# Optimization experiments

Hardware: AMD Instinct MI355X
Metric: run time of the kernel (lower is better)

Reference implementation:

```python
import jax, jax.numpy as jnp
import numpy as np

B, L, D, H, MAXREL = 8, 1024, 1024, 16, 32
DPH = D // H  # 64


def setup_inputs() -> dict:
    rng = jax.random.key(0)
    ks = jax.random.split(rng, 16)
    s = 0.02
    inp = {
        "key": jax.random.normal(ks[0], (B, L, D), jnp.float32),
        "value": jax.random.normal(ks[1], (B, L, D), jnp.float32),
        "query": jax.random.normal(ks[2], (B, L, D), jnp.float32),
        "mask": jax.random.bernoulli(ks[3], 0.1, (B, 1, L)),
        "Wq": jax.random.normal(ks[4], (D, D), jnp.float32) * s,
        "bq": jnp.zeros((D,), jnp.float32),
        "Wk": jax.random.normal(ks[5], (D, D), jnp.float32) * s,
        "bk": jnp.zeros((D,), jnp.float32),
        "Wv": jax.random.normal(ks[6], (D, D), jnp.float32) * s,
        "bv": jnp.zeros((D,), jnp.float32),
        "Wo": jax.random.normal(ks[7], (D, D), jnp.float32) * s,
        "bo": jnp.zeros((D,), jnp.float32),
        "rel_emb": jax.random.normal(ks[8], (2 * MAXREL + 1, DPH), jnp.float32) * s,
    }
    return inp


def reference(key, value, query, mask, Wq, bq, Wk, bk, Wv, bv, Wo, bo, rel_emb):
    b, l, d = query.shape
    def shape(x):  # (b, l, D) -> (b, H, l, dph)
        return x.reshape(b, -1, H, DPH).transpose(0, 2, 1, 3)

    q = shape(query @ Wq.T + bq) / jnp.sqrt(jnp.asarray(DPH, query.dtype))
    k = shape(key @ Wk.T + bk)
    v = shape(value @ Wv.T + bv)

    # Shaw-style relative position embeddings: rel[i, j] = clip(j - i, -M, M) + M
    idx = jnp.arange(l)
    rel = jnp.clip(idx[None, :] - idx[:, None], -MAXREL, MAXREL) + MAXREL  # (l, l)
    Er = rel_emb[rel]  # (l, l, dph) -- used for both keys and values (same table)

    scores = jnp.einsum('bhqd,bhkd->bhqk', q, k) + jnp.einsum('bhqd,qkd->bhqk', q, Er)
    scores = jnp.where(mask[:, None, :, :], jnp.asarray(-1e18, scores.dtype), scores)
    attn = jax.nn.softmax(scores, axis=-1)  # dropout = identity at eval

    ctx = jnp.einsum('bhqk,bhkd->bhqd', attn, v) + jnp.einsum('bhqk,qkd->bhqd', attn, Er)
    out = ctx.transpose(0, 2, 1, 3).reshape(b, l, H * DPH) @ Wo.T + bo
    top_attn = attn[:, 0]  # (b, q_len, k_len)
    return out, top_attn
```

## Files before the change

### kernel.cpp

```cpp
#include <hip/hip_runtime.h>
#include <hip/hip_bf16.h>

typedef __bf16 bf16x8 __attribute__((ext_vector_type(8)));
typedef __bf16 bf16x4 __attribute__((ext_vector_type(4)));
typedef float f32x4 __attribute__((ext_vector_type(4)));
typedef float f32x8 __attribute__((ext_vector_type(8)));

#define B_ 8
#define L_ 1024
#define D_ 1024
#define H_ 16
#define DPH_ 64
#define MAXREL_ 32
#define NREL_ 65

__device__ __forceinline__ f32x4 mfma16x16x32(bf16x8 a, bf16x8 b, f32x4 c) {
    return __builtin_amdgcn_mfma_f32_16x16x32_bf16(a, b, c, 0, 0, 0);
}

__device__ __forceinline__ bf16x8 ld_any(const float* p) {
    f32x8 v = *(const f32x8*)p;
    bf16x8 r;
    #pragma unroll
    for (int i = 0; i < 8; ++i) r[i] = (__bf16)v[i];
    return r;
}
__device__ __forceinline__ bf16x8 ld_any(const __bf16* p) { return *(const bf16x8*)p; }

template <int MODE, typename TA>
__global__ __launch_bounds__(256) void gemm128(
    const TA* __restrict__ X, const float* __restrict__ Wt,
    const float* __restrict__ bias, void* __restrict__ outp,
    int M, int N, int K, float scale)
{
    __shared__ __bf16 sA[128 * 64];
    __shared__ __bf16 sB[128 * 64];

    const int tid = threadIdx.x;
    const int nbn = N >> 7;
    const int nwg = (M >> 7) * nbn;
    const int wg  = ((int)blockIdx.x & 7) * (nwg >> 3) + ((int)blockIdx.x >> 3);
    const int row0 = (wg / nbn) * 128, col0 = (wg % nbn) * 128;
    const int lane = tid & 63, w = tid >> 6, lr = lane & 15, lk = lane >> 4;
    const int wm = w >> 1, wn = w & 1;
    const int srow = tid >> 3;
    const int schk = tid & 7;

    bf16x8 ra[4], rb[4];
    f32x4 acc[4][4];
    #pragma unroll
    for (int a = 0; a < 4; ++a)
        #pragma unroll
        for (int b = 0; b < 4; ++b) acc[a][b] = (f32x4){0.f, 0.f, 0.f, 0.f};

    const int nkt = K >> 6;
    {
        const int kc = schk * 8;
        #pragma unroll
        for (int u = 0; u < 4; ++u) {
            const int r = u * 32 + srow;
            ra[u] = ld_any(X  + (size_t)(row0 + r) * K + kc);
            rb[u] = ld_any(Wt + (size_t)(col0 + r) * K + kc);
        }
    }
    for (int kt = 0; kt < nkt; ++kt) {
        __syncthreads();
        #pragma unroll
        for (int u = 0; u < 4; ++u) {
            const int r = u * 32 + srow;
            *(bf16x8*)&sA[r * 64 + ((schk ^ (r & 7)) * 8)] = ra[u];
            *(bf16x8*)&sB[r * 64 + ((schk ^ (r & 7)) * 8)] = rb[u];
        }
        __syncthreads();
        if (kt + 1 < nkt) {
            const int kc = (kt + 1) * 64 + schk * 8;
            #pragma unroll
            for (int u = 0; u < 4; ++u) {
                const int r = u * 32 + srow;
                ra[u] = ld_any(X  + (size_t)(row0 + r) * K + kc);
                rb[u] = ld_any(Wt + (size_t)(col0 + r) * K + kc);
            }
        }
        #pragma unroll
        for (int kk = 0; kk < 2; ++kk) {
            bf16x8 af[4], bf[4];
            #pragma unroll
            for (int mi = 0; mi < 4; ++mi) {
                const int r = wm * 64 + mi * 16 + lr;
                af[mi] = *(const bf16x8*)&sA[r * 64 + (((kk * 4 + lk) ^ (r & 7)) * 8)];
            }
            #pragma unroll
            for (int ni = 0; ni < 4; ++ni) {
                const int r = wn * 64 + ni * 16 + lr;
                bf[ni] = *(const bf16x8*)&sB[r * 64 + (((kk * 4 + lk) ^ (r & 7)) * 8)];
            }
            #pragma unroll
            for (int mi = 0; mi < 4; ++mi)
                #pragma unroll
                for (int ni = 0; ni < 4; ++ni)
                    acc[mi][ni] = mfma16x16x32(af[mi], bf[ni], acc[mi][ni]);
        }
    }

    #pragma unroll
    for (int ni = 0; ni < 4; ++ni) {
        const int n = col0 + wn * 64 + ni * 16 + lr;
        const float bv = bias[n];
        #pragma unroll
        for (int mi = 0; mi < 4; ++mi) {
            const int m0 = row0 + wm * 64 + mi * 16 + lk * 4;
            if (MODE == 0) {
                #pragma unroll
                for (int i = 0; i < 4; ++i)
                    ((__bf16*)outp)[(size_t)(m0 + i) * N + n] =
                        (__bf16)((acc[mi][ni][i] + bv) * scale);
            } else if (MODE == 1) {
                bf16x4 v4;
                #pragma unroll
                for (int i = 0; i < 4; ++i) v4[i] = (__bf16)(acc[mi][ni][i] + bv);
                *(bf16x4*)((__bf16*)outp + ((size_t)(m0 >> 10) << 20)
                           + (size_t)n * L_ + (m0 & 1023)) = v4;
            } else {
                #pragma unroll
                for (int i = 0; i < 4; ++i)
                    ((float*)outp)[(size_t)(m0 + i) * N + n] = acc[mi][ni][i] + bv;
            }
        }
    }
}

__global__ __launch_bounds__(256, 3) void attn_v5(
    const __bf16* __restrict__ Q, const __bf16* __restrict__ K,
    const __bf16* __restrict__ Vt, const int* __restrict__ mask,
    const float* __restrict__ relg, __bf16* __restrict__ ctx,
    float* __restrict__ attn0)
{
    __shared__ __bf16 sK[2][64 * 64];
    __shared__ __bf16 sV[2][64 * 64];
    __shared__ __bf16 s_rq[64 * 72];
    __shared__ __bf16 s_arel[64 * 72];
    __shared__ float s_sums[64];
    __shared__ unsigned s_mbits[32];

    const int tid = threadIdx.x;
    const int wg = ((int)blockIdx.x & 7) * 256 + ((int)blockIdx.x >> 3);
    const int qt = wg & 15, h = (wg >> 4) & 15, b = wg >> 8;
    const int q0 = qt * 64;
    const int lane = tid & 63, w = tid >> 6, lr = lane & 15, lk = lane >> 4;
    const size_t bh = (size_t)b * (L_ * D_) + (size_t)h * DPH_;
    const int qw = q0 + w * 16;
    const int ql = w * 16;

    const int strow = tid >> 3;
    const int scg   = (tid & 7) ^ (strow & 7);
    const __bf16* Kgp = K + bh + (size_t)strow * D_ + scg * 8;
    const __bf16* Vgp = Vt + ((size_t)b << 20)
                      + (size_t)(h * DPH_ + strow) * L_ + scg * 8;

    const __bf16* qp = Q + bh + (size_t)(qw + lr) * D_ + 8 * lk;
    const bf16x8 qf0 = *(const bf16x8*)qp;
    const bf16x8 qf1 = *(const bf16x8*)(qp + 32);

    #pragma unroll
    for (int rr = 0; rr < 4; ++rr) {
        const int k = rr * 256 + w * 64 + lane;
        const unsigned long long bal = __ballot(mask[b * L_ + k] != 0);
        if (lane == 0) {
            s_mbits[rr * 8 + w * 2]     = (unsigned)bal;
            s_mbits[rr * 8 + w * 2 + 1] = (unsigned)(bal >> 32);
        }
    }
    for (int i = tid; i < 64 * 72; i += 256) s_arel[i] = (__bf16)0.f;

    #pragma unroll
    for (int jt = 0; jt < 5; ++jt) {
        const int jr = jt * 16 + lr;
        const int jc = jr > 64 ? 64 : jr;
        const float* rp = relg + jc * 64 + 8 * lk;
        f32x4 rq = {0.f, 0.f, 0.f, 0.f};
        rq = mfma16x16x32(ld_any(rp), qf0, rq);
        rq = mfma16x16x32(ld_any(rp + 32), qf1, rq);
        #pragma unroll
        for (int i = 0; i < 4; ++i) {
            const int jj = jt * 16 + lk * 4 + i;
            if (jj <= 64) s_rq[(ql + lr) * 72 + jj] = (__bf16)rq[i];
        }
    }

    bf16x8 rk0 = *(const bf16x8*)(Kgp);
    bf16x8 rk1 = *(const bf16x8*)(Kgp + 32 * (size_t)D_);
    bf16x8 rv0 = *(const bf16x8*)(Vgp);
    bf16x8 rv1 = *(const bf16x8*)(Vgp + 32 * (size_t)L_);
    __syncthreads();

    const float rq0  = (float)s_rq[(ql + lr) * 72 + 0];
    const float rq64 = (float)s_rq[(ql + lr) * 72 + 64];

    float sum = 0.f, c0 = 0.f, c64 = 0.f;
    f32x4 pvacc[4];
    #pragma unroll
    for (int dt = 0; dt < 4; ++dt) pvacc[dt] = (f32x4){0.f, 0.f, 0.f, 0.f};
    float* a0p = attn0 + ((size_t)b * L_ + qw + lr) * L_;
    const int sw = lr & 7;
    const int s0l = lr + 32 * (lk & 1);
    const int s1l = s0l + 16;
    const bool hisel = (lk >> 1) != 0;

    for (int it = 0; it < 16; ++it) {
        const int cur = it & 1;
        const int k0 = it * 64;
        {
            __bf16* kd = &sK[cur][tid * 8];
            __bf16* vd = &sV[cur][tid * 8];
            *(bf16x8*)kd = rk0;  *(bf16x8*)(kd + 2048) = rk1;
            *(bf16x8*)vd = rv0;  *(bf16x8*)(vd + 2048) = rv1;
        }
        __syncthreads();
        if (it < 15) {
            const size_t ko = (size_t)(k0 + 64) * D_;
            rk0 = *(const bf16x8*)(Kgp + ko);
            rk1 = *(const bf16x8*)(Kgp + ko + 32 * (size_t)D_);
            rv0 = *(const bf16x8*)(Vgp + k0 + 64);
            rv1 = *(const bf16x8*)(Vgp + k0 + 64 + 32 * (size_t)L_);
        }

        const __bf16* kb = sK[cur];
        const __bf16* vb = sV[cur];

        float p[4][4];
        #pragma unroll
        for (int kt = 0; kt < 4; ++kt) {
            const int rb = (kt * 16 + lr) * 64;
            const bf16x8 a0 = *(const bf16x8*)&kb[rb + ((lk ^ sw) * 8)];
            const bf16x8 a1 = *(const bf16x8*)&kb[rb + (((lk + 4) ^ sw) * 8)];
            f32x4 acc = {0.f, 0.f, 0.f, 0.f};
            acc = mfma16x16x32(a0, qf0, acc);
            acc = mfma16x16x32(a1, qf1, acc);
            #pragma unroll
            for (int i = 0; i < 4; ++i) p[kt][i] = acc[i];
        }

        const unsigned mw0 = s_mbits[(k0 >> 5)];
        const unsigned mw1 = s_mbits[(k0 >> 5) + 1];
        const int side = (k0 <= qw - 95) ? -1 : ((k0 >= qw + 47) ? 1 : 0);
        if (side == 0) {
            #pragma unroll
            for (int kt = 0; kt < 4; ++kt) {
                const unsigned mword = kt < 2 ? mw0 : mw1;
                #pragma unroll
                for (int i = 0; i < 4; ++i) {
                    const int k = k0 + kt * 16 + lk * 4 + i;
                    const int dd = k - (qw + lr);
                    int j = dd + MAXREL_;
                    j = j < 0 ? 0 : (j > 64 ? 64 : j);
                    const float bias = (float)s_rq[(ql + lr) * 72 + j];
                    const float e = ((mword >> (k & 31)) & 1u)
                                  ? 0.f : __expf(p[kt][i] + bias);
                    p[kt][i] = e;
                    sum += e;
                    if (dd <= -MAXREL_)      c0  += e;
                    else if (dd >= MAXREL_)  c64 += e;
                    else s_arel[(ql + lr) * 72 + dd + MAXREL_] = (__bf16)e;
                }
            }
        } else {
            const float bias = side < 0 ? rq0 : rq64;
            float cacc = 0.f;
            #pragma unroll
            for (int kt = 0; kt < 4; ++kt) {
                const unsigned mword = kt < 2 ? mw0 : mw1;
                #pragma unroll
                for (int i = 0; i < 4; ++i) {
                    const int k = k0 + kt * 16 + lk * 4 + i;
                    const float e = ((mword >> (k & 31)) & 1u)
                                  ? 0.f : __expf(p[kt][i] + bias);
                    p[kt][i] = e;
                    cacc += e;
                }
            }
            sum += cacc;
            if (side < 0) c0 += cacc; else c64 += cacc;
        }

        if (h == 0) {
            #pragma unroll
            for (int kt = 0; kt < 4; ++kt) {
                f32x4 st;
                #pragma unroll
                for (int i = 0; i < 4; ++i) st[i] = p[kt][i];
                *(f32x4*)&a0p[k0 + kt * 16 + lk * 4] = st;
            }
        }

        unsigned pk[4][2];
        #pragma unroll
        for (int kt = 0; kt < 4; ++kt)
            #pragma unroll
            for (int hf = 0; hf < 2; ++hf) {
                union { unsigned u; __bf16 x[2]; } t;
                t.x[0] = (__bf16)p[kt][2 * hf];
                t.x[1] = (__bf16)p[kt][2 * hf + 1];
                pk[kt][hf] = t.u;
            }

        #pragma unroll
        for (int s = 0; s < 2; ++s) {
            union { unsigned u[4]; bf16x8 v; } ua;
            {
                const unsigned aE0 = __shfl((int)pk[2 * s][0],     s0l, 64);
                const unsigned aO0 = __shfl((int)pk[2 * s + 1][0], s0l, 64);
                const unsigned aE1 = __shfl((int)pk[2 * s][1],     s0l, 64);
                const unsigned aO1 = __shfl((int)pk[2 * s + 1][1], s0l, 64);
                const unsigned bE0 = __shfl((int)pk[2 * s][0],     s1l, 64);
                const unsigned bO0 = __shfl((int)pk[2 * s + 1][0], s1l, 64);
                const unsigned bE1 = __shfl((int)pk[2 * s][1],     s1l, 64);
                const unsigned bO1 = __shfl((int)pk[2 * s + 1][1], s1l, 64);
                ua.u[0] = hisel ? aO0 : aE0;
                ua.u[1] = hisel ? aO1 : aE1;
                ua.u[2] = hisel ? bO0 : bE0;
                ua.u[3] = hisel ? bO1 : bE1;
            }
            #pragma unroll
            for (int dt = 0; dt < 4; ++dt) {
                const bf16x8 bfv = *(const bf16x8*)
                    &vb[(dt * 16 + lr) * 64 + (((4 * s + lk) ^ sw) * 8)];
                pvacc[dt] = mfma16x16x32(ua.v, bfv, pvacc[dt]);
            }
        }
    }

    sum += __shfl_xor(sum, 16, 64); sum += __shfl_xor(sum, 32, 64);
    c0  += __shfl_xor(c0, 16, 64);  c0  += __shfl_xor(c0, 32, 64);
    c64 += __shfl_xor(c64, 16, 64); c64 += __shfl_xor(c64, 32, 64);
    if (lane < 16) {
        s_sums[ql + lr] = sum;
        s_arel[(ql + lr) * 72 + 0]  = (__bf16)c0;
        s_arel[(ql + lr) * 72 + 64] = (__bf16)c64;
    }
    __syncthreads();

    __bf16* rT = (__bf16*)sK;
    for (int i = tid; i < NREL_ * DPH_; i += 256)
        rT[(i & 63) * 72 + (i >> 6)] = (__bf16)relg[i];
    __syncthreads();

    const bf16x8 af1 = *(const bf16x8*)&s_arel[(ql + lr) * 72 + 8 * lk];
    const bf16x8 af2 = *(const bf16x8*)&s_arel[(ql + lr) * 72 + 32 + 8 * lk];
    float a64[4], inv[4];
    #pragma unroll
    for (int i = 0; i < 4; ++i) {
        a64[i] = (float)s_arel[(ql + lk * 4 + i) * 72 + 64];
        inv[i] = 1.f / s_sums[ql + lk * 4 + i];
    }
    #pragma unroll
    for (int dt = 0; dt < 4; ++dt) {
        const bf16x8 b1 = *(const bf16x8*)&rT[(dt * 16 + lr) * 72 + 8 * lk];
        const bf16x8 b2 = *(const bf16x8*)&rT[(dt * 16 + lr) * 72 + 32 + 8 * lk];
        pvacc[dt] = mfma16x16x32(af1, b1, pvacc[dt]);
        pvacc[dt] = mfma16x16x32(af2, b2, pvacc[dt]);
        const float r64 = (float)rT[(dt * 16 + lr) * 72 + 64];
        #pragma unroll
        for (int i = 0; i < 4; ++i) {
            const float outv = (pvacc[dt][i] + a64[i] * r64) * inv[i];
            ctx[((size_t)b * L_ + q0 + ql + lk * 4 + i) * D_
                + h * DPH_ + dt * 16 + lr] = (__bf16)outv;
        }
    }

    if (h == 0) {
        #pragma unroll 4
        for (int n = 0; n < 16; ++n) {
            const float invr = 1.f / s_sums[ql + n];
            float* ap = attn0 + ((size_t)b * L_ + q0 + ql + n) * L_ + lane * 16;
            #pragma unroll
            for (int c = 0; c < 4; ++c) {
                f32x4 v = *(f32x4*)&ap[c * 4];
                #pragma unroll
                for (int i = 0; i < 4; ++i) v[i] *= invr;
                *(f32x4*)&ap[c * 4] = v;
            }
        }
    }
}

extern "C" void kernel_launch(void* const* d_in, const int* in_sizes, int n_in,
                              void* d_out, int out_size, void* d_ws, size_t ws_size,
                              hipStream_t stream) {
    const float* key   = (const float*)d_in[0];
    const float* value = (const float*)d_in[1];
    const float* query = (const float*)d_in[2];
    const int*   mask  = (const int*)d_in[3];
    const float* Wq = (const float*)d_in[4];
    const float* bq = (const float*)d_in[5];
    const float* Wk = (const float*)d_in[6];
    const float* bk = (const float*)d_in[7];
    const float* Wv = (const float*)d_in[8];
    const float* bv = (const float*)d_in[9];
    const float* Wo = (const float*)d_in[10];
    const float* bo = (const float*)d_in[11];
    const float* relg = (const float*)d_in[12];

    float* out   = (float*)d_out;
    float* attn0 = out + (size_t)B_ * L_ * D_;

    char* ws = (char*)d_ws;
    __bf16* Qw   = (__bf16*)(ws);
    __bf16* Kw   = (__bf16*)(ws + ((size_t)16 << 20));
    __bf16* Vtw  = (__bf16*)(ws + ((size_t)32 << 20));
    __bf16* Ctxw = (__bf16*)(ws + ((size_t)48 << 20));

    const dim3 blk(256);
    const int M = B_ * L_;
    const int ngemm = (M / 128) * (D_ / 128);

    gemm128<0, float><<<ngemm, blk, 0, stream>>>(query, Wq, bq, Qw, M, D_, D_, 0.125f);
    gemm128<0, float><<<ngemm, blk, 0, stream>>>(key,   Wk, bk, Kw, M, D_, D_, 1.0f);
    gemm128<1, float><<<ngemm, blk, 0, stream>>>(value, Wv, bv, Vtw, M, D_, D_, 1.0f);

    attn_v5<<<B_ * H_ * (L_ / 64), blk, 0, stream>>>(
        Qw, Kw, Vtw, mask, relg, Ctxw, attn0);

    gemm128<2, __bf16><<<ngemm, blk, 0, stream>>>(Ctxw, Wo, bo, out, M, D_, D_, 1.0f);
}
```

Baseline: 238.3 us.

## Rewrite projection GEMMs with 128x256 tiles, double-buffered LDS and 512 threads

The projection GEMM kernel is replaced by a version that uses 128x256 output tiles with 8 waves, K-steps of 32 and double-buffered shared memory, so each iteration needs only one barrier and global loads run two steps ahead. LDS rows are padded to 40 elements instead of XOR-swizzled, and MFMA issue is wrapped in s_setprio. The aim is to overlap global loads with MFMA work and cut synchronisation. In exchange, the grid has half as many blocks, the tile-index swizzle is dropped, and padded LDS reads may cause some bank conflicts.

```diff
diff --git a/kernel.cpp b/kernel.cpp
--- a/kernel.cpp
+++ b/kernel.cpp
@@ -28,79 +28,99 @@
 __device__ __forceinline__ bf16x8 ld_any(const __bf16* p) { return *(const bf16x8*)p; }
 
 template <int MODE, typename TA>
-__global__ __launch_bounds__(256) void gemm128(
+__global__ __launch_bounds__(512, 2) void gemm_v2(
     const TA* __restrict__ X, const float* __restrict__ Wt,
     const float* __restrict__ bias, void* __restrict__ outp,
     int M, int N, int K, float scale)
 {
-    __shared__ __bf16 sA[128 * 64];
-    __shared__ __bf16 sB[128 * 64];
+    __shared__ __bf16 sA[2][128 * 40];
+    __shared__ __bf16 sB[2][256 * 40];
 
     const int tid = threadIdx.x;
-    const int nbn = N >> 7;
-    const int nwg = (M >> 7) * nbn;
-    const int wg  = ((int)blockIdx.x & 7) * (nwg >> 3) + ((int)blockIdx.x >> 3);
-    const int row0 = (wg / nbn) * 128, col0 = (wg % nbn) * 128;
+    const int nbn = N >> 8;
+    const int wg = (int)blockIdx.x;
+    const int row0 = (wg / nbn) * 128, col0 = (wg % nbn) * 256;
     const int lane = tid & 63, w = tid >> 6, lr = lane & 15, lk = lane >> 4;
-    const int wm = w >> 1, wn = w & 1;
-    const int srow = tid >> 3;
-    const int schk = tid & 7;
-
-    bf16x8 ra[4], rb[4];
+    const int wm = w >> 2, wn = w & 3;
+
+    const int arow = tid >> 2, ak = (tid & 3) * 8;
+    const int brow = tid >> 1, bk = (tid & 1) * 16;
+    const TA*    agp = X  + (size_t)(row0 + arow) * K + ak;
+    const float* bgp = Wt + (size_t)(col0 + brow) * K + bk;
+
     f32x4 acc[4][4];
     #pragma unroll
     for (int a = 0; a < 4; ++a)
         #pragma unroll
         for (int b = 0; b < 4; ++b) acc[a][b] = (f32x4){0.f, 0.f, 0.f, 0.f};
 
-    const int nkt = K >> 6;
-    {
-        const int kc = schk * 8;
-        #pragma unroll
-        for (int u = 0; u < 4; ++u) {
-            const int r = u * 32 + srow;
-            ra[u] = ld_any(X  + (size_t)(row0 + r) * K + kc);
-            rb[u] = ld_any(Wt + (size_t)(col0 + r) * K + kc);
-        }
-    }
-    for (int kt = 0; kt < nkt; ++kt) {
-        __syncthreads();
-        #pragma unroll
-        for (int u = 0; u < 4; ++u) {
-            const int r = u * 32 + srow;
-            *(bf16x8*)&sA[r * 64 + ((schk ^ (r & 7)) * 8)] = ra[u];
-            *(bf16x8*)&sB[r * 64 + ((schk ^ (r & 7)) * 8)] = rb[u];
-        }
-        __syncthreads();
-        if (kt + 1 < nkt) {
-            const int kc = (kt + 1) * 64 + schk * 8;
-            #pragma unroll
-            for (int u = 0; u < 4; ++u) {
-                const int r = u * 32 + srow;
-                ra[u] = ld_any(X  + (size_t)(row0 + r) * K + kc);
-                rb[u] = ld_any(Wt + (size_t)(col0 + r) * K + kc);
-            }
-        }
-        #pragma unroll
-        for (int kk = 0; kk < 2; ++kk) {
-            bf16x8 af[4], bf[4];
-            #pragma unroll
-            for (int mi = 0; mi < 4; ++mi) {
-                const int r = wm * 64 + mi * 16 + lr;
-                af[mi] = *(const bf16x8*)&sA[r * 64 + (((kk * 4 + lk) ^ (r & 7)) * 8)];
-            }
-            #pragma unroll
-            for (int ni = 0; ni < 4; ++ni) {
-                const int r = wn * 64 + ni * 16 + lr;
-                bf[ni] = *(const bf16x8*)&sB[r * 64 + (((kk * 4 + lk) ^ (r & 7)) * 8)];
-            }
-            #pragma unroll
-            for (int mi = 0; mi < 4; ++mi)
-                #pragma unroll
-                for (int ni = 0; ni < 4; ++ni)
-                    acc[mi][ni] = mfma16x16x32(af[mi], bf[ni], acc[mi][ni]);
-        }
-    }
+    f32x4 ra0, ra1;
+    bf16x8 rab;
+    f32x4 rb0, rb1, rb2, rb3;
+
+    #define LOADG(t) do {                                                    \
+        const int _k0 = (t) * 32;                                            \
+        if (sizeof(TA) == 4) {                                               \
+            ra0 = *(const f32x4*)((const float*)agp + _k0);                  \
+            ra1 = *(const f32x4*)((const float*)agp + _k0 + 4);              \
+        } else {                                                             \
+            rab = *(const bf16x8*)((const __bf16*)agp + _k0);                \
+        }                                                                    \
+        rb0 = *(const f32x4*)(bgp + _k0);                                    \
+        rb1 = *(const f32x4*)(bgp + _k0 + 4);                                \
+        rb2 = *(const f32x4*)(bgp + _k0 + 8);                                \
+        rb3 = *(const f32x4*)(bgp + _k0 + 12);                               \
+    } while (0)
+
+    #define WRITEL(buf) do {                                                 \
+        bf16x8 _av;                                                          \
+        if (sizeof(TA) == 4) {                                               \
+            _Pragma("unroll")                                                \
+            for (int i = 0; i < 4; ++i) {                                    \
+                _av[i] = (__bf16)ra0[i]; _av[4 + i] = (__bf16)ra1[i];        \
+            }                                                                \
+        } else { _av = rab; }                                                \
+        *(bf16x8*)&sA[buf][arow * 40 + ak] = _av;                            \
+        bf16x8 _bv0, _bv1;                                                   \
+        _Pragma("unroll")                                                    \
+        for (int i = 0; i < 4; ++i) {                                        \
+            _bv0[i] = (__bf16)rb0[i]; _bv0[4 + i] = (__bf16)rb1[i];          \
+            _bv1[i] = (__bf16)rb2[i]; _bv1[4 + i] = (__bf16)rb3[i];          \
+        }                                                                    \
+        *(bf16x8*)&sB[buf][brow * 40 + bk]     = _bv0;                       \
+        *(bf16x8*)&sB[buf][brow * 40 + bk + 8] = _bv1;                       \
+    } while (0)
+
+    LOADG(0);
+    WRITEL(0);
+    LOADG(1);
+    __syncthreads();
+
+    const int nkt = K >> 5;
+    for (int t = 0; t < nkt; ++t) {
+        const int cur = t & 1;
+        bf16x8 af[4], bfr[4];
+        #pragma unroll
+        for (int m = 0; m < 4; ++m)
+            af[m] = *(const bf16x8*)&sA[cur][(wm * 64 + m * 16 + lr) * 40 + 8 * lk];
+        #pragma unroll
+        for (int n = 0; n < 4; ++n)
+            bfr[n] = *(const bf16x8*)&sB[cur][(wn * 64 + n * 16 + lr) * 40 + 8 * lk];
+        __builtin_amdgcn_s_setprio(1);
+        #pragma unroll
+        for (int m = 0; m < 4; ++m)
+            #pragma unroll
+            for (int n = 0; n < 4; ++n)
+                acc[m][n] = mfma16x16x32(af[m], bfr[n], acc[m][n]);
+        __builtin_amdgcn_s_setprio(0);
+        if (t < nkt - 1) {
+            WRITEL(cur ^ 1);
+            if (t < nkt - 2) LOADG(t + 2);
+            __syncthreads();
+        }
+    }
+    #undef LOADG
+    #undef WRITEL
 
     #pragma unroll
     for (int ni = 0; ni < 4; ++ni) {
@@ -409,16 +429,15 @@
     __bf16* Vtw  = (__bf16*)(ws + ((size_t)32 << 20));
     __bf16* Ctxw = (__bf16*)(ws + ((size_t)48 << 20));
 
-    const dim3 blk(256);
     const int M = B_ * L_;
-    const int ngemm = (M / 128) * (D_ / 128);
-
-    gemm128<0, float><<<ngemm, blk, 0, stream>>>(query, Wq, bq, Qw, M, D_, D_, 0.125f);
-    gemm128<0, float><<<ngemm, blk, 0, stream>>>(key,   Wk, bk, Kw, M, D_, D_, 1.0f);
-    gemm128<1, float><<<ngemm, blk, 0, stream>>>(value, Wv, bv, Vtw, M, D_, D_, 1.0f);
-
-    attn_v5<<<B_ * H_ * (L_ / 64), blk, 0, stream>>>(
+    const int ngemm = (M / 128) * (D_ / 256);
+
+    gemm_v2<0, float><<<ngemm, dim3(512), 0, stream>>>(query, Wq, bq, Qw, M, D_, D_, 0.125f);
+    gemm_v2<0, float><<<ngemm, dim3(512), 0, stream>>>(key,   Wk, bk, Kw, M, D_, D_, 1.0f);
+    gemm_v2<1, float><<<ngemm, dim3(512), 0, stream>>>(value, Wv, bv, Vtw, M, D_, D_, 1.0f);
+
+    attn_v5<<<B_ * H_ * (L_ / 64), dim3(256), 0, stream>>>(
         Qw, Kw, Vtw, mask, relg, Ctxw, attn0);
 
-    gemm128<2, __bf16><<<ngemm, blk, 0, stream>>>(Ctxw, Wo, bo, out, M, D_, D_, 1.0f);
+    gemm_v2<2, __bf16><<<ngemm, dim3(512), 0, stream>>>(Ctxw, Wo, bo, out, M, D_, D_, 1.0f);
 }
```

Result: no change. 240.5 us (+0.9%).
